# Kernel tuning notes

Measured on AMD Instinct MI355X. Metric: run time of the kernel, lower is better.

Reference implementation:

```python
import jax, jax.numpy as jnp
import numpy as np

# graph constants
B, V, CG, K, H, IN = 4, 6250, 25000, 3, 64, 2
NUM_LIT = B * 2 * V          # 50_000 literal nodes
NUM_CLS = B * CG             # 100_000 clause nodes
E = K * NUM_CLS              # 300_000 (l2c, c2l) edge pairs
NUM_ROUND = 3
DEMON = float(np.sqrt(H))    # self.demon = sqrt(hidden_size)


def setup_inputs() -> dict:
    key = jax.random.key(0)
    ks = jax.random.split(key, 12)
    rng = np.random.default_rng(0)
    # each clause has K literal endpoints; edges stay inside their own graph
    cls_idx = np.repeat(np.arange(NUM_CLS), K)
    g = cls_idx // CG
    lit_idx = g * 2 * V + rng.integers(0, 2 * V, size=E)

    def lin(k, fi, fo):
        return (jax.random.normal(k, (fi, fo), jnp.float32) / np.sqrt(fi)).astype(jnp.float32)

    return {
        "feat_l2c": jax.random.normal(ks[0], (E, IN), jnp.float32),
        "feat_c2l": jax.random.normal(ks[1], (E, IN), jnp.float32),
        "lit_idx": jnp.asarray(lit_idx, jnp.int32),
        "cls_idx": jnp.asarray(cls_idx, jnp.int32),
        "W_l2c_init": lin(ks[2], IN, H), "b_l2c_init": jnp.zeros((H,), jnp.float32),
        "W_c2l_init": lin(ks[3], IN, H), "b_c2l_init": jnp.zeros((H,), jnp.float32),
        "msgl_W": (jax.random.normal(ks[4], (3, H, H), jnp.float32) / np.sqrt(H)).astype(jnp.float32),
        "msgl_b": jnp.zeros((3, H), jnp.float32),
        "merge_W0": lin(ks[5], 2 * H, H), "merge_b0": jnp.zeros((H,), jnp.float32),
        "merge_Wr": (jax.random.normal(ks[6], (2, H, H), jnp.float32) / np.sqrt(H)).astype(jnp.float32),
        "merge_br": jnp.zeros((2, H), jnp.float32),
        "msgc_W": (jax.random.normal(ks[7], (3, H, H), jnp.float32) / np.sqrt(H)).astype(jnp.float32),
        "msgc_b": jnp.zeros((3, H), jnp.float32),
        "ro_W": (jax.random.normal(ks[8], (2, H, H), jnp.float32) / np.sqrt(H)).astype(jnp.float32),
        "ro_b": jnp.zeros((2, H), jnp.float32),
        "ro_W2": lin(ks[9], H, 1), "ro_b2": jnp.zeros((1,), jnp.float32),
    }


def _mlp3(x, W, b):  # 3-layer MLP, ReLU between layers (num_fc = 3)
    x = jax.nn.relu(x @ W[0] + b[0])
    x = jax.nn.relu(x @ W[1] + b[1])
    return x @ W[2] + b[2]


def reference(feat_l2c, feat_c2l, lit_idx, cls_idx,
              W_l2c_init, b_l2c_init, W_c2l_init, b_c2l_init,
              msgl_W, msgl_b, merge_W0, merge_b0, merge_Wr, merge_br,
              msgc_W, msgc_b, ro_W, ro_b, ro_W2, ro_b2):
    # init edge embeddings (l2c_init / c2l_init linear layers)
    h_l2c = feat_l2c @ W_l2c_init + b_l2c_init   # [E, H]
    h_c2l = feat_c2l @ W_c2l_init + b_c2l_init   # [E, H]

    for _ in range(NUM_ROUND):
        # literal update: aggregate incoming c2l messages, exclude self edge (BP-style)
        agg_l = jax.ops.segment_sum(h_c2l, lit_idx, num_segments=NUM_LIT)   # [NUM_LIT, H]
        m = _mlp3((agg_l[lit_idx] - h_c2l) / DEMON, msgl_W, msgl_b)          # [E, H]
        x = jax.nn.relu(jnp.concatenate([m, h_l2c], axis=-1) @ merge_W0 + merge_b0)
        x = jax.nn.relu(x @ merge_Wr[0] + merge_br[0])
        h_l2c = x @ merge_Wr[1] + merge_br[1]                                # l2c_merge_update
        # clause update
        agg_c = jax.ops.segment_sum(h_l2c, cls_idx, num_segments=NUM_CLS)   # [NUM_CLS, H]
        h_c2l = _mlp3((agg_c[cls_idx] - h_l2c) / DEMON, msgc_W, msgc_b)

    # u_add_e_sum with zero node feats == scatter-add edge emb to dst;
    # literal nodes only receive c2l edges
    l_emb = jax.ops.segment_sum(h_c2l, lit_idx, num_segments=NUM_LIT)        # [NUM_LIT, H]
    # segment_reduce(num_variable*2, ..., 'mean') over per-graph literal blocks (uniform sizes)
    l_mean = l_emb.reshape(B, 2 * V, H).mean(axis=1)                          # [B, H]
    x = jax.nn.relu(l_mean @ ro_W[0] + ro_b[0])
    x = jax.nn.relu(x @ ro_W[1] + ro_b[1])
    return jax.nn.sigmoid(x @ ro_W2 + ro_b2).squeeze(-1)                      # [B]
```

## Files before the change

kernel.cpp:

```cpp
#include <hip/hip_runtime.h>
#include <hip/hip_bf16.h>
#include <stdint.h>

#define EDGES   300000
#define NLIT    50000
#define NGRAPH  4
#define EPG     75000
#define HDIM    64

#define OFF_HL2C   0
#define OFF_HC2L   38400000
#define OFF_AGG    76800000
#define OFF_WT     89600000
#define OFF_ROACC  89681920
#define OFF_CNT    89682944
#define OFF_CSROFF 89882944
#define OFF_CURSOR 90082948
#define OFF_EIDX   90282948
#define OFF_BSUM   91482948
#define OFF_BBASE  91484000

#define WT_TOTAL    40960
#define WT_CLS_ELEM 28672

#define LIT_WBYTES (7 * 8192)
#define CLS_WBYTES (3 * 8192)
#define EPB2       256
#define NCHUNK     ((EDGES + EPB2 - 1) / EPB2)
#define LIT_GRID   512
#define CLS_GRID   1024

#define SCAN_BLOCKS ((NLIT + 255) / 256)

typedef __attribute__((ext_vector_type(8)))  short          s16x8;
typedef __attribute__((ext_vector_type(8)))  unsigned short u16x8;
typedef __attribute__((ext_vector_type(4)))  unsigned short u16x4;
typedef __attribute__((ext_vector_type(4)))  float          f32x4;
typedef __attribute__((ext_vector_type(16))) float          f32x16;

__device__ __forceinline__ f32x16 mfma32(s16x8 a, s16x8 b, f32x16 c) {
    return __builtin_amdgcn_mfma_f32_32x32x16_bf16(a, b, c, 0, 0, 0);
}
__device__ __forceinline__ float bf2f(unsigned short s) {
    union { unsigned int u; float f; } v; v.u = ((unsigned int)s) << 16; return v.f;
}
__device__ __forceinline__ unsigned short f2bf(float f) {
    union { __hip_bfloat16 b; unsigned short s; } v;
    v.b = __float2bfloat16(f);
    return v.s;
}
__device__ __forceinline__ unsigned pk2(float a, float b) {
    return (unsigned)f2bf(a) | ((unsigned)f2bf(b) << 16);
}

__device__ __forceinline__ void layer32(const char* __restrict__ unitBase,
                                        const float* __restrict__ biasL,
                                        const s16x8 (&bin)[4], f32x16 (&acc)[2],
                                        int eL, int hi)
{
#pragma unroll
    for (int t = 0; t < 2; ++t)
#pragma unroll
        for (int g = 0; g < 4; ++g) {
            f32x4 bv = *(const f32x4*)(biasL + 32 * t + 8 * g + 4 * hi);
#pragma unroll
            for (int r = 0; r < 4; ++r) acc[t][4 * g + r] = bv[r];
        }
#pragma unroll
    for (int kb = 0; kb < 4; ++kb)
#pragma unroll
        for (int t = 0; t < 2; ++t) {
            int row = 32 * t + eL;
            s16x8 a = *(const s16x8*)(unitBase + row * 128 +
                                      ((32 * kb + 16 * hi) ^ ((row & 7) << 4)));
            acc[t] = mfma32(a, bin[kb], acc[t]);
        }
}

template<bool RELU>
__device__ __forceinline__ void relayout32(f32x16 (&acc)[2], s16x8 (&bout)[4],
                                           int bpidx, int hi)
{
    if (RELU) {
#pragma unroll
        for (int t = 0; t < 2; ++t)
#pragma unroll
            for (int i = 0; i < 16; ++i) acc[t][i] = fmaxf(acc[t][i], 0.f);
    }
#pragma unroll
    for (int kb = 0; kb < 4; ++kb) {
        int m0 = 2 * kb, m1 = 2 * kb + 1;
        int t0 = m0 >> 2, g0 = m0 & 3, t1 = m1 >> 2, g1 = m1 & 3;
        unsigned A0 = pk2(acc[t0][4 * g0 + 0], acc[t0][4 * g0 + 1]);
        unsigned A1 = pk2(acc[t0][4 * g0 + 2], acc[t0][4 * g0 + 3]);
        unsigned B0 = pk2(acc[t1][4 * g1 + 0], acc[t1][4 * g1 + 1]);
        unsigned B1 = pk2(acc[t1][4 * g1 + 2], acc[t1][4 * g1 + 3]);
        unsigned pA0 = (unsigned)__builtin_amdgcn_ds_bpermute(bpidx, (int)A0);
        unsigned pA1 = (unsigned)__builtin_amdgcn_ds_bpermute(bpidx, (int)A1);
        unsigned pB0 = (unsigned)__builtin_amdgcn_ds_bpermute(bpidx, (int)B0);
        unsigned pB1 = (unsigned)__builtin_amdgcn_ds_bpermute(bpidx, (int)B1);
        union { unsigned w[4]; s16x8 v; } u;
        u.w[0] = hi ? pB0 : A0;
        u.w[1] = hi ? pB1 : A1;
        u.w[2] = hi ? B0 : pA0;
        u.w[3] = hi ? B1 : pA1;
        bout[kb] = u.v;
    }
}

__device__ __forceinline__ void store32(const f32x16 (&acc)[2],
                                        unsigned short* __restrict__ dst, int hi)
{
#pragma unroll
    for (int t = 0; t < 2; ++t)
#pragma unroll
        for (int g = 0; g < 4; ++g) {
            u16x4 p;
#pragma unroll
            for (int r = 0; r < 4; ++r) p[r] = f2bf(acc[t][4 * g + r]);
            *(u16x4*)(dst + 32 * t + 8 * g + 4 * hi) = p;
        }
}

__global__ __launch_bounds__(256) void prep_weights(
    const float* __restrict__ msgl_W, const float* __restrict__ merge_W0,
    const float* __restrict__ merge_Wr, const float* __restrict__ msgc_W,
    unsigned short* __restrict__ wT)
{
    int gid = blockIdx.x * 256 + threadIdx.x;
    if (gid >= WT_TOTAL) return;
    int unit = gid >> 12;
    int o = (gid >> 6) & 63;
    int csw = gid & 63;
    int i = csw ^ ((o & 7) << 3);
    float v;
    if (unit < 3)       v = msgl_W[unit * 4096 + i * 64 + o];
    else if (unit < 5)  v = merge_W0[((unit - 3) * 64 + i) * 64 + o];
    else if (unit < 7)  v = merge_Wr[(unit - 5) * 4096 + i * 64 + o];
    else                v = msgc_W[(unit - 7) * 4096 + i * 64 + o];
    wT[gid] = f2bf(v);
}

__global__ __launch_bounds__(256) void csr_hist(const int* __restrict__ lit_idx,
                                                int* __restrict__ cnt)
{
    int e = blockIdx.x * 256 + threadIdx.x;
    if (e < EDGES) atomicAdd(&cnt[lit_idx[e]], 1);
}

__global__ __launch_bounds__(256) void scan1(const int* __restrict__ cnt,
                                             int* __restrict__ bsum)
{
    __shared__ int red[4];
    int i = blockIdx.x * 256 + threadIdx.x;
    int s = (i < NLIT) ? cnt[i] : 0;
#pragma unroll
    for (int off = 1; off < 64; off <<= 1) s += __shfl_xor(s, off, 64);
    if ((threadIdx.x & 63) == 0) red[threadIdx.x >> 6] = s;
    __syncthreads();
    if (threadIdx.x == 0) bsum[blockIdx.x] = red[0] + red[1] + red[2] + red[3];
}

__global__ __launch_bounds__(256) void scan2(const int* __restrict__ bsum,
                                             int* __restrict__ bbase)
{
    __shared__ int tmp[256];
    int t = threadIdx.x;
    int v = (t < SCAN_BLOCKS) ? bsum[t] : 0;
    tmp[t] = v;
    __syncthreads();
#pragma unroll
    for (int off = 1; off < 256; off <<= 1) {
        int add = (t >= off) ? tmp[t - off] : 0;
        __syncthreads();
        tmp[t] += add;
        __syncthreads();
    }
    if (t < SCAN_BLOCKS) bbase[t] = tmp[t] - v;
}

__global__ __launch_bounds__(256) void scan3(const int* __restrict__ cnt,
                                             const int* __restrict__ bbase,
                                             int* __restrict__ off,
                                             int* __restrict__ cursor)
{
    __shared__ int tmp[256];
    int t = threadIdx.x;
    int i = blockIdx.x * 256 + t;
    int v = (i < NLIT) ? cnt[i] : 0;
    tmp[t] = v;
    __syncthreads();
#pragma unroll
    for (int offs = 1; offs < 256; offs <<= 1) {
        int add = (t >= offs) ? tmp[t - offs] : 0;
        __syncthreads();
        tmp[t] += add;
        __syncthreads();
    }
    if (i < NLIT) {
        int ex = bbase[blockIdx.x] + tmp[t] - v;
        off[i] = ex; cursor[i] = ex;
    }
    if (i == NLIT - 1) off[NLIT] = EDGES;
}

__global__ __launch_bounds__(256) void csr_scatter(const int* __restrict__ lit_idx,
                                                   int* __restrict__ cursor,
                                                   int* __restrict__ eidx)
{
    int e = blockIdx.x * 256 + threadIdx.x;
    if (e >= EDGES) return;
    int pos = atomicAdd(&cursor[lit_idx[e]], 1);
    eidx[pos] = e;
}

__global__ __launch_bounds__(256) void aggregate(const unsigned short* __restrict__ h_c2l,
                                                 const int* __restrict__ off,
                                                 const int* __restrict__ eidx,
                                                 float* __restrict__ agg)
{
    int t = threadIdx.x;
    int lane8 = t & 7;
    int lit = blockIdx.x * 32 + (t >> 3);
    if (lit >= NLIT) return;
    int lo = off[lit], hi = off[lit + 1];
    float s[8] = {0, 0, 0, 0, 0, 0, 0, 0};
    for (int i = lo; i < hi; ++i) {
        int e = eidx[i];
        u16x8 hv = *(const u16x8*)(h_c2l + e * 64 + lane8 * 8);
#pragma unroll
        for (int j = 0; j < 8; ++j) s[j] += bf2f(hv[j]);
    }
    f32x4 a0, a1;
    a0[0] = s[0]; a0[1] = s[1]; a0[2] = s[2]; a0[3] = s[3];
    a1[0] = s[4]; a1[1] = s[5]; a1[2] = s[6]; a1[3] = s[7];
    *(f32x4*)(agg + lit * 64 + lane8 * 8)     = a0;
    *(f32x4*)(agg + lit * 64 + lane8 * 8 + 4) = a1;
}

__global__ __launch_bounds__(256) void init_kernel(
    const float* __restrict__ feat_l2c, const float* __restrict__ feat_c2l,
    const float* __restrict__ W_l2c, const float* __restrict__ b_l2c,
    const float* __restrict__ W_c2l, const float* __restrict__ b_c2l,
    unsigned short* __restrict__ h_l2c, unsigned short* __restrict__ h_c2l)
{
    int gid = blockIdx.x * 256 + threadIdx.x;
    if (gid >= EDGES * 8) return;
    int e = gid >> 3, fo = (gid & 7) << 3;
    float2 fl = *(const float2*)(feat_l2c + e * 2);
    float2 fc = *(const float2*)(feat_c2l + e * 2);

    u16x8 outl, outc;
#pragma unroll
    for (int j = 0; j < 8; ++j) {
        float wl0 = W_l2c[fo + j], wl1 = W_l2c[64 + fo + j];
        float wc0 = W_c2l[fo + j], wc1 = W_c2l[64 + fo + j];
        float vl = fl.x * wl0 + fl.y * wl1 + b_l2c[fo + j];
        float vc = fc.x * wc0 + fc.y * wc1 + b_c2l[fo + j];
        outl[j] = f2bf(vl);
        outc[j] = f2bf(vc);
    }
    *(u16x8*)(h_l2c + e * 64 + fo) = outl;
    *(u16x8*)(h_c2l + e * 64 + fo) = outc;
}

__global__ __launch_bounds__(512, 4) void lit_update(
    const unsigned short* __restrict__ h_c2l,
    unsigned short* __restrict__ h_l2c,
    const float* __restrict__ agg,
    const int* __restrict__ lit_idx,
    const unsigned short* __restrict__ wT,
    const float* __restrict__ msgl_b,
    const float* __restrict__ merge_b0,
    const float* __restrict__ merge_br)
{
    __shared__ __align__(16) char lds[LIT_WBYTES + 384 * 4];
    int tid = threadIdx.x;
#pragma unroll
    for (int c = 0; c < 7; ++c) {
        int idx = c * 512 + tid;
        *(u16x8*)(lds + idx * 16) = *(const u16x8*)(wT + idx * 8);
    }
    float* ldsBias = (float*)(lds + LIT_WBYTES);
    if (tid < 384) {
        float v;
        if (tid < 192)      v = msgl_b[tid];
        else if (tid < 256) v = merge_b0[tid - 192];
        else                v = merge_br[tid - 256];
        ldsBias[tid] = v;
    }
    __syncthreads();

    int wv = tid >> 6, lane = tid & 63;
    int eL = lane & 31, hi = lane >> 5;
    int bpidx = (lane ^ 32) << 2;

    for (int c = blockIdx.x; c < NCHUNK; c += LIT_GRID) {
        int base = c * EPB2 + wv * 32;
        if (base >= EDGES) continue;
        int e = base + eL;
        int lit = lit_idx[e];

        s16x8 hfrag[4];
#pragma unroll
        for (int k = 0; k < 4; ++k)
            hfrag[k] = *(const s16x8*)(h_l2c + e * 64 + 16 * k + 8 * hi);

        s16x8 binp[4];
#pragma unroll
        for (int k = 0; k < 4; ++k) {
            int f0 = 16 * k + 8 * hi;
            f32x4 a0 = *(const f32x4*)(agg + lit * 64 + f0);
            f32x4 a1 = *(const f32x4*)(agg + lit * 64 + f0 + 4);
            u16x8 hv = *(const u16x8*)(h_c2l + e * 64 + f0);
            s16x8 b;
#pragma unroll
            for (int j = 0; j < 4; ++j) b[j]     = (short)f2bf((a0[j] - bf2f(hv[j]))     * 0.125f);
#pragma unroll
            for (int j = 0; j < 4; ++j) b[4 + j] = (short)f2bf((a1[j] - bf2f(hv[4 + j])) * 0.125f);
            binp[k] = b;
        }

        f32x16 acc[2];
        s16x8 bf[4];
        layer32(lds,            ldsBias,       binp, acc, eL, hi);
        relayout32<true >(acc, bf, bpidx, hi);
        layer32(lds + 8192,     ldsBias + 64,  bf, acc, eL, hi);
        relayout32<true >(acc, bf, bpidx, hi);
        layer32(lds + 2 * 8192, ldsBias + 128, bf, acc, eL, hi);
        relayout32<false>(acc, bf, bpidx, hi);

#pragma unroll
        for (int t = 0; t < 2; ++t)
#pragma unroll
            for (int g = 0; g < 4; ++g) {
                f32x4 bv = *(const f32x4*)(ldsBias + 192 + 32 * t + 8 * g + 4 * hi);
#pragma unroll
                for (int r = 0; r < 4; ++r) acc[t][4 * g + r] = bv[r];
            }
#pragma unroll
        for (int kb = 0; kb < 8; ++kb) {
            const char* ub = lds + (3 + (kb >> 2)) * 8192;
            s16x8 bop = (kb < 4) ? bf[kb] : hfrag[kb - 4];
#pragma unroll
            for (int t = 0; t < 2; ++t) {
                int row = 32 * t + eL;
                s16x8 a = *(const s16x8*)(ub + row * 128 +
                                          ((32 * (kb & 3) + 16 * hi) ^ ((row & 7) << 4)));
                acc[t] = mfma32(a, bop, acc[t]);
            }
        }
        relayout32<true>(acc, bf, bpidx, hi);
        layer32(lds + 5 * 8192, ldsBias + 256, bf, acc, eL, hi);
        relayout32<true>(acc, bf, bpidx, hi);
        layer32(lds + 6 * 8192, ldsBias + 320, bf, acc, eL, hi);

        store32(acc, h_l2c + e * 64, hi);
    }
}

__global__ __launch_bounds__(512, 4) void clause_update(
    const unsigned short* __restrict__ h_l2c,
    unsigned short* __restrict__ h_c2l,
    const unsigned short* __restrict__ msgcT,
    const float* __restrict__ msgc_b)
{
    __shared__ __align__(16) char lds[CLS_WBYTES + 192 * 4];
    int tid = threadIdx.x;
#pragma unroll
    for (int c = 0; c < 3; ++c) {
        int idx = c * 512 + tid;
        *(u16x8*)(lds + idx * 16) = *(const u16x8*)(msgcT + idx * 8);
    }
    float* ldsBias = (float*)(lds + CLS_WBYTES);
    if (tid < 192) ldsBias[tid] = msgc_b[tid];
    __syncthreads();

    int wv = tid >> 6, lane = tid & 63;
    int eL = lane & 31, hi = lane >> 5;
    int bpidx = (lane ^ 32) << 2;

    for (int c = blockIdx.x; c < NCHUNK; c += CLS_GRID) {
        int base = c * EPB2 + wv * 32;
        if (base >= EDGES) continue;
        int e = base + eL;

        int c3 = (e / 3) * 3;
        int d = e - c3;
        int e1 = c3 + (d == 0 ? 1 : 0);
        int e2 = c3 + (d == 2 ? 1 : 2);

        s16x8 binp[4];
#pragma unroll
        for (int k = 0; k < 4; ++k) {
            int f0 = 16 * k + 8 * hi;
            u16x8 h1 = *(const u16x8*)(h_l2c + e1 * 64 + f0);
            u16x8 h2 = *(const u16x8*)(h_l2c + e2 * 64 + f0);
            s16x8 b;
#pragma unroll
            for (int j = 0; j < 8; ++j)
                b[j] = (short)f2bf((bf2f(h1[j]) + bf2f(h2[j])) * 0.125f);
            binp[k] = b;
        }

        f32x16 acc[2];
        s16x8 bf[4];
        layer32(lds,            ldsBias,       binp, acc, eL, hi);
        relayout32<true>(acc, bf, bpidx, hi);
        layer32(lds + 8192,     ldsBias + 64,  bf, acc, eL, hi);
        relayout32<true>(acc, bf, bpidx, hi);
        layer32(lds + 2 * 8192, ldsBias + 128, bf, acc, eL, hi);

        store32(acc, h_c2l + e * 64, hi);
    }
}

__global__ __launch_bounds__(256) void readout_sum(
    const unsigned short* __restrict__ h_c2l, float* __restrict__ ro_acc)
{
    __shared__ float lsum[32][64];
    int g = blockIdx.x >> 6, chunk = blockIdx.x & 63;
    int t = threadIdx.x;
    int fg = t & 7, el = t >> 3;
    float s[8] = {0, 0, 0, 0, 0, 0, 0, 0};
    for (int idx = chunk * 32 + el; idx < EPG; idx += 2048) {
        u16x8 hv = *(const u16x8*)(h_c2l + (g * EPG + idx) * 64 + fg * 8);
#pragma unroll
        for (int j = 0; j < 8; ++j) s[j] += bf2f(hv[j]);
    }
#pragma unroll
    for (int j = 0; j < 8; ++j) lsum[el][fg * 8 + j] = s[j];
    __syncthreads();
    if (t < 64) {
        float tot = 0.f;
#pragma unroll 8
        for (int r = 0; r < 32; ++r) tot += lsum[r][t];
        atomicAdd(&ro_acc[g * 64 + t], tot);
    }
}

__global__ __launch_bounds__(256) void readout_mlp(
    const float* __restrict__ ro_acc, const float* __restrict__ ro_W,
    const float* __restrict__ ro_b, const float* __restrict__ ro_W2,
    const float* __restrict__ ro_b2, float* __restrict__ out)
{
    __shared__ float xb[NGRAPH][HDIM];
    __shared__ float yb[NGRAPH][HDIM];
    int g = threadIdx.x >> 6;
    int j = threadIdx.x & 63;
    xb[g][j] = ro_acc[g * HDIM + j] * (1.0f / 12500.0f);
    __syncthreads();
    float a = ro_b[j];
#pragma unroll 8
    for (int k = 0; k < HDIM; ++k) a += xb[g][k] * ro_W[k * HDIM + j];
    a = fmaxf(a, 0.0f);
    yb[g][j] = a;
    __syncthreads();
    float a2 = ro_b[HDIM + j];
#pragma unroll 8
    for (int k = 0; k < HDIM; ++k) a2 += yb[g][k] * ro_W[4096 + k * HDIM + j];
    a2 = fmaxf(a2, 0.0f);
    float p = a2 * ro_W2[j];
#pragma unroll
    for (int off = 32; off > 0; off >>= 1) p += __shfl_down(p, off, 64);
    if (j == 0) out[g] = 1.0f / (1.0f + expf(-(p + ro_b2[0])));
}

extern "C" void kernel_launch(void* const* d_in, const int* in_sizes, int n_in,
                              void* d_out, int out_size, void* d_ws, size_t ws_size,
                              hipStream_t stream)
{
    const float* feat_l2c = (const float*)d_in[0];
    const float* feat_c2l = (const float*)d_in[1];
    const int*   lit_idx  = (const int*)d_in[2];
    const float* W_l2c    = (const float*)d_in[4];
    const float* b_l2c    = (const float*)d_in[5];
    const float* W_c2l    = (const float*)d_in[6];
    const float* b_c2l    = (const float*)d_in[7];
    const float* msgl_W   = (const float*)d_in[8];
    const float* msgl_b   = (const float*)d_in[9];
    const float* merge_W0 = (const float*)d_in[10];
    const float* merge_b0 = (const float*)d_in[11];
    const float* merge_Wr = (const float*)d_in[12];
    const float* merge_br = (const float*)d_in[13];
    const float* msgc_W   = (const float*)d_in[14];
    const float* msgc_b   = (const float*)d_in[15];
    const float* ro_W     = (const float*)d_in[16];
    const float* ro_b     = (const float*)d_in[17];
    const float* ro_W2    = (const float*)d_in[18];
    const float* ro_b2    = (const float*)d_in[19];

    char* ws = (char*)d_ws;
    unsigned short* h_l2c  = (unsigned short*)(ws + OFF_HL2C);
    unsigned short* h_c2l  = (unsigned short*)(ws + OFF_HC2L);
    float*          agg    = (float*)(ws + OFF_AGG);
    unsigned short* wT     = (unsigned short*)(ws + OFF_WT);
    float*          ro_acc = (float*)(ws + OFF_ROACC);
    int*            cnt    = (int*)(ws + OFF_CNT);
    int*            csroff = (int*)(ws + OFF_CSROFF);
    int*            cursor = (int*)(ws + OFF_CURSOR);
    int*            eidx   = (int*)(ws + OFF_EIDX);
    int*            bsum   = (int*)(ws + OFF_BSUM);
    int*            bbase  = (int*)(ws + OFF_BBASE);

    hipMemsetAsync(cnt, 0, NLIT * sizeof(int), stream);
    hipMemsetAsync(ro_acc, 0, NGRAPH * 64 * sizeof(float), stream);

    prep_weights<<<(WT_TOTAL + 255) / 256, 256, 0, stream>>>(msgl_W, merge_W0, merge_Wr, msgc_W, wT);

    csr_hist<<<(EDGES + 255) / 256, 256, 0, stream>>>(lit_idx, cnt);
    scan1<<<SCAN_BLOCKS, 256, 0, stream>>>(cnt, bsum);
    scan2<<<1, 256, 0, stream>>>(bsum, bbase);
    scan3<<<SCAN_BLOCKS, 256, 0, stream>>>(cnt, bbase, csroff, cursor);
    csr_scatter<<<(EDGES + 255) / 256, 256, 0, stream>>>(lit_idx, cursor, eidx);

    init_kernel<<<EDGES * 8 / 256, 256, 0, stream>>>(feat_l2c, feat_c2l, W_l2c, b_l2c,
                                                     W_c2l, b_c2l, h_l2c, h_c2l);
    for (int r = 0; r < 3; ++r) {
        aggregate<<<(NLIT + 31) / 32, 256, 0, stream>>>(h_c2l, csroff, eidx, agg);
        lit_update<<<LIT_GRID, 512, 0, stream>>>(h_c2l, h_l2c, agg, lit_idx, wT,
                                                 msgl_b, merge_b0, merge_br);
        clause_update<<<CLS_GRID, 512, 0, stream>>>(h_l2c, h_c2l, wT + WT_CLS_ELEM, msgc_b);
    }
    readout_sum<<<256, 256, 0, stream>>>(h_c2l, ro_acc);
    readout_mlp<<<1, 256, 0, stream>>>(ro_acc, ro_W, ro_b, ro_W2, ro_b2, (float*)d_out);
}
```

Measured before the change: 341.6 us.

## Process two edge tiles per wave in lit_update and flatten grid loops

lit_update now has each wave handle two 32-edge tiles, sharing every LDS weight fragment load across two MFMA chains. Its launch bound drops to 3 blocks per CU to make room for the extra registers. Both update kernels switch from grid-stride loops to one chunk per block with a larger grid. relayout32 halves its ds_bpermute count by selecting the value to send before the permute, and the aggregate gather loop is unrolled by four to put more loads in flight. The higher register pressure in lit_update may lower occupancy or cause spills.

```diff
diff --git a/kernel.cpp b/kernel.cpp
--- a/kernel.cpp
+++ b/kernel.cpp
@@ -25,10 +25,10 @@
 
 #define LIT_WBYTES (7 * 8192)
 #define CLS_WBYTES (3 * 8192)
-#define EPB2       256
-#define NCHUNK     ((EDGES + EPB2 - 1) / EPB2)
-#define LIT_GRID   512
-#define CLS_GRID   1024
+#define LIT_EPB    512
+#define LIT_GRID   ((EDGES + LIT_EPB - 1) / LIT_EPB)
+#define CLS_EPB    256
+#define CLS_GRID   ((EDGES + CLS_EPB - 1) / CLS_EPB)
 
 #define SCAN_BLOCKS ((NLIT + 255) / 256)
 
@@ -51,30 +51,6 @@
 }
 __device__ __forceinline__ unsigned pk2(float a, float b) {
     return (unsigned)f2bf(a) | ((unsigned)f2bf(b) << 16);
-}
-
-__device__ __forceinline__ void layer32(const char* __restrict__ unitBase,
-                                        const float* __restrict__ biasL,
-                                        const s16x8 (&bin)[4], f32x16 (&acc)[2],
-                                        int eL, int hi)
-{
-#pragma unroll
-    for (int t = 0; t < 2; ++t)
-#pragma unroll
-        for (int g = 0; g < 4; ++g) {
-            f32x4 bv = *(const f32x4*)(biasL + 32 * t + 8 * g + 4 * hi);
-#pragma unroll
-            for (int r = 0; r < 4; ++r) acc[t][4 * g + r] = bv[r];
-        }
-#pragma unroll
-    for (int kb = 0; kb < 4; ++kb)
-#pragma unroll
-        for (int t = 0; t < 2; ++t) {
-            int row = 32 * t + eL;
-            s16x8 a = *(const s16x8*)(unitBase + row * 128 +
-                                      ((32 * kb + 16 * hi) ^ ((row & 7) << 4)));
-            acc[t] = mfma32(a, bin[kb], acc[t]);
-        }
 }
 
 template<bool RELU>
@@ -95,15 +71,15 @@
         unsigned A1 = pk2(acc[t0][4 * g0 + 2], acc[t0][4 * g0 + 3]);
         unsigned B0 = pk2(acc[t1][4 * g1 + 0], acc[t1][4 * g1 + 1]);
         unsigned B1 = pk2(acc[t1][4 * g1 + 2], acc[t1][4 * g1 + 3]);
-        unsigned pA0 = (unsigned)__builtin_amdgcn_ds_bpermute(bpidx, (int)A0);
-        unsigned pA1 = (unsigned)__builtin_amdgcn_ds_bpermute(bpidx, (int)A1);
-        unsigned pB0 = (unsigned)__builtin_amdgcn_ds_bpermute(bpidx, (int)B0);
-        unsigned pB1 = (unsigned)__builtin_amdgcn_ds_bpermute(bpidx, (int)B1);
+        unsigned s0 = hi ? A0 : B0;
+        unsigned s1 = hi ? A1 : B1;
+        unsigned p0 = (unsigned)__builtin_amdgcn_ds_bpermute(bpidx, (int)s0);
+        unsigned p1 = (unsigned)__builtin_amdgcn_ds_bpermute(bpidx, (int)s1);
         union { unsigned w[4]; s16x8 v; } u;
-        u.w[0] = hi ? pB0 : A0;
-        u.w[1] = hi ? pB1 : A1;
-        u.w[2] = hi ? B0 : pA0;
-        u.w[3] = hi ? B1 : pA1;
+        u.w[0] = hi ? p0 : A0;
+        u.w[1] = hi ? p1 : A1;
+        u.w[2] = hi ? B0 : p0;
+        u.w[3] = hi ? B1 : p1;
         bout[kb] = u.v;
     }
 }
@@ -119,6 +95,56 @@
 #pragma unroll
             for (int r = 0; r < 4; ++r) p[r] = f2bf(acc[t][4 * g + r]);
             *(u16x4*)(dst + 32 * t + 8 * g + 4 * hi) = p;
+        }
+}
+
+__device__ __forceinline__ void layer32(const char* __restrict__ unitBase,
+                                        const float* __restrict__ biasL,
+                                        const s16x8 (&bin)[4], f32x16 (&acc)[2],
+                                        int eL, int hi)
+{
+#pragma unroll
+    for (int t = 0; t < 2; ++t)
+#pragma unroll
+        for (int g = 0; g < 4; ++g) {
+            f32x4 bv = *(const f32x4*)(biasL + 32 * t + 8 * g + 4 * hi);
+#pragma unroll
+            for (int r = 0; r < 4; ++r) acc[t][4 * g + r] = bv[r];
+        }
+#pragma unroll
+    for (int kb = 0; kb < 4; ++kb)
+#pragma unroll
+        for (int t = 0; t < 2; ++t) {
+            int row = 32 * t + eL;
+            s16x8 a = *(const s16x8*)(unitBase + row * 128 +
+                                      ((32 * kb + 16 * hi) ^ ((row & 7) << 4)));
+            acc[t] = mfma32(a, bin[kb], acc[t]);
+        }
+}
+
+__device__ __forceinline__ void layer32x2(const char* __restrict__ unitBase,
+                                          const float* __restrict__ biasL,
+                                          const s16x8 (&b0)[4], const s16x8 (&b1)[4],
+                                          f32x16 (&acc0)[2], f32x16 (&acc1)[2],
+                                          int eL, int hi)
+{
+#pragma unroll
+    for (int t = 0; t < 2; ++t)
+#pragma unroll
+        for (int g = 0; g < 4; ++g) {
+            f32x4 bv = *(const f32x4*)(biasL + 32 * t + 8 * g + 4 * hi);
+#pragma unroll
+            for (int r = 0; r < 4; ++r) { acc0[t][4 * g + r] = bv[r]; acc1[t][4 * g + r] = bv[r]; }
+        }
+#pragma unroll
+    for (int kb = 0; kb < 4; ++kb)
+#pragma unroll
+        for (int t = 0; t < 2; ++t) {
+            int row = 32 * t + eL;
+            s16x8 a = *(const s16x8*)(unitBase + row * 128 +
+                                      ((32 * kb + 16 * hi) ^ ((row & 7) << 4)));
+            acc0[t] = mfma32(a, b0[kb], acc0[t]);
+            acc1[t] = mfma32(a, b1[kb], acc1[t]);
         }
 }
 
@@ -225,7 +251,18 @@
     if (lit >= NLIT) return;
     int lo = off[lit], hi = off[lit + 1];
     float s[8] = {0, 0, 0, 0, 0, 0, 0, 0};
-    for (int i = lo; i < hi; ++i) {
+    int i = lo;
+    for (; i + 4 <= hi; i += 4) {
+        int e0 = eidx[i], e1 = eidx[i + 1], e2 = eidx[i + 2], e3 = eidx[i + 3];
+        u16x8 v0 = *(const u16x8*)(h_c2l + e0 * 64 + lane8 * 8);
+        u16x8 v1 = *(const u16x8*)(h_c2l + e1 * 64 + lane8 * 8);
+        u16x8 v2 = *(const u16x8*)(h_c2l + e2 * 64 + lane8 * 8);
+        u16x8 v3 = *(const u16x8*)(h_c2l + e3 * 64 + lane8 * 8);
+#pragma unroll
+        for (int j = 0; j < 8; ++j)
+            s[j] += (bf2f(v0[j]) + bf2f(v1[j])) + (bf2f(v2[j]) + bf2f(v3[j]));
+    }
+    for (; i < hi; ++i) {
         int e = eidx[i];
         u16x8 hv = *(const u16x8*)(h_c2l + e * 64 + lane8 * 8);
 #pragma unroll
@@ -264,7 +301,7 @@
     *(u16x8*)(h_c2l + e * 64 + fo) = outc;
 }
 
-__global__ __launch_bounds__(512, 4) void lit_update(
+__global__ __launch_bounds__(512, 3) void lit_update(
     const unsigned short* __restrict__ h_c2l,
     unsigned short* __restrict__ h_l2c,
     const float* __restrict__ agg,
@@ -294,69 +331,86 @@
     int wv = tid >> 6, lane = tid & 63;
     int eL = lane & 31, hi = lane >> 5;
     int bpidx = (lane ^ 32) << 2;
-
-    for (int c = blockIdx.x; c < NCHUNK; c += LIT_GRID) {
-        int base = c * EPB2 + wv * 32;
-        if (base >= EDGES) continue;
-        int e = base + eL;
-        int lit = lit_idx[e];
-
-        s16x8 hfrag[4];
-#pragma unroll
-        for (int k = 0; k < 4; ++k)
-            hfrag[k] = *(const s16x8*)(h_l2c + e * 64 + 16 * k + 8 * hi);
-
-        s16x8 binp[4];
-#pragma unroll
-        for (int k = 0; k < 4; ++k) {
-            int f0 = 16 * k + 8 * hi;
-            f32x4 a0 = *(const f32x4*)(agg + lit * 64 + f0);
-            f32x4 a1 = *(const f32x4*)(agg + lit * 64 + f0 + 4);
-            u16x8 hv = *(const u16x8*)(h_c2l + e * 64 + f0);
-            s16x8 b;
-#pragma unroll
-            for (int j = 0; j < 4; ++j) b[j]     = (short)f2bf((a0[j] - bf2f(hv[j]))     * 0.125f);
-#pragma unroll
-            for (int j = 0; j < 4; ++j) b[4 + j] = (short)f2bf((a1[j] - bf2f(hv[4 + j])) * 0.125f);
-            binp[k] = b;
-        }
-
-        f32x16 acc[2];
-        s16x8 bf[4];
-        layer32(lds,            ldsBias,       binp, acc, eL, hi);
-        relayout32<true >(acc, bf, bpidx, hi);
-        layer32(lds + 8192,     ldsBias + 64,  bf, acc, eL, hi);
-        relayout32<true >(acc, bf, bpidx, hi);
-        layer32(lds + 2 * 8192, ldsBias + 128, bf, acc, eL, hi);
-        relayout32<false>(acc, bf, bpidx, hi);
-
-#pragma unroll
-        for (int t = 0; t < 2; ++t)
-#pragma unroll
-            for (int g = 0; g < 4; ++g) {
-                f32x4 bv = *(const f32x4*)(ldsBias + 192 + 32 * t + 8 * g + 4 * hi);
-#pragma unroll
-                for (int r = 0; r < 4; ++r) acc[t][4 * g + r] = bv[r];
-            }
-#pragma unroll
-        for (int kb = 0; kb < 8; ++kb) {
-            const char* ub = lds + (3 + (kb >> 2)) * 8192;
-            s16x8 bop = (kb < 4) ? bf[kb] : hfrag[kb - 4];
-#pragma unroll
-            for (int t = 0; t < 2; ++t) {
-                int row = 32 * t + eL;
-                s16x8 a = *(const s16x8*)(ub + row * 128 +
-                                          ((32 * (kb & 3) + 16 * hi) ^ ((row & 7) << 4)));
-                acc[t] = mfma32(a, bop, acc[t]);
-            }
-        }
-        relayout32<true>(acc, bf, bpidx, hi);
-        layer32(lds + 5 * 8192, ldsBias + 256, bf, acc, eL, hi);
-        relayout32<true>(acc, bf, bpidx, hi);
-        layer32(lds + 6 * 8192, ldsBias + 320, bf, acc, eL, hi);
-
-        store32(acc, h_l2c + e * 64, hi);
-    }
+    int base = blockIdx.x * LIT_EPB + wv * 64;
+    if (base >= EDGES) return;
+    bool has2 = (base + 32) < EDGES;
+    int e0 = base + eL;
+    int e1 = has2 ? (base + 32 + eL) : e0;
+    int l0 = lit_idx[e0];
+    int l1 = lit_idx[e1];
+
+    s16x8 hfragA[4], hfragB[4];
+#pragma unroll
+    for (int k = 0; k < 4; ++k) {
+        hfragA[k] = *(const s16x8*)(h_l2c + e0 * 64 + 16 * k + 8 * hi);
+        hfragB[k] = *(const s16x8*)(h_l2c + e1 * 64 + 16 * k + 8 * hi);
+    }
+
+    s16x8 bfA[4], bfB[4];
+#pragma unroll
+    for (int k = 0; k < 4; ++k) {
+        int f0 = 16 * k + 8 * hi;
+        f32x4 a0 = *(const f32x4*)(agg + l0 * 64 + f0);
+        f32x4 a1 = *(const f32x4*)(agg + l0 * 64 + f0 + 4);
+        u16x8 hv = *(const u16x8*)(h_c2l + e0 * 64 + f0);
+        s16x8 b;
+#pragma unroll
+        for (int j = 0; j < 4; ++j) b[j]     = (short)f2bf((a0[j] - bf2f(hv[j]))     * 0.125f);
+#pragma unroll
+        for (int j = 0; j < 4; ++j) b[4 + j] = (short)f2bf((a1[j] - bf2f(hv[4 + j])) * 0.125f);
+        bfA[k] = b;
+        f32x4 c0 = *(const f32x4*)(agg + l1 * 64 + f0);
+        f32x4 c1 = *(const f32x4*)(agg + l1 * 64 + f0 + 4);
+        u16x8 hw = *(const u16x8*)(h_c2l + e1 * 64 + f0);
+#pragma unroll
+        for (int j = 0; j < 4; ++j) b[j]     = (short)f2bf((c0[j] - bf2f(hw[j]))     * 0.125f);
+#pragma unroll
+        for (int j = 0; j < 4; ++j) b[4 + j] = (short)f2bf((c1[j] - bf2f(hw[4 + j])) * 0.125f);
+        bfB[k] = b;
+    }
+
+    f32x16 accA[2], accB[2];
+    layer32x2(lds,            ldsBias,       bfA, bfB, accA, accB, eL, hi);
+    relayout32<true >(accA, bfA, bpidx, hi);
+    relayout32<true >(accB, bfB, bpidx, hi);
+    layer32x2(lds + 8192,     ldsBias + 64,  bfA, bfB, accA, accB, eL, hi);
+    relayout32<true >(accA, bfA, bpidx, hi);
+    relayout32<true >(accB, bfB, bpidx, hi);
+    layer32x2(lds + 2 * 8192, ldsBias + 128, bfA, bfB, accA, accB, eL, hi);
+    relayout32<false>(accA, bfA, bpidx, hi);
+    relayout32<false>(accB, bfB, bpidx, hi);
+
+#pragma unroll
+    for (int t = 0; t < 2; ++t)
+#pragma unroll
+        for (int g = 0; g < 4; ++g) {
+            f32x4 bv = *(const f32x4*)(ldsBias + 192 + 32 * t + 8 * g + 4 * hi);
+#pragma unroll
+            for (int r = 0; r < 4; ++r) { accA[t][4 * g + r] = bv[r]; accB[t][4 * g + r] = bv[r]; }
+        }
+#pragma unroll
+    for (int kb = 0; kb < 8; ++kb) {
+        const char* ub = lds + (3 + (kb >> 2)) * 8192;
+        s16x8 bA = (kb < 4) ? bfA[kb] : hfragA[kb - 4];
+        s16x8 bB = (kb < 4) ? bfB[kb] : hfragB[kb - 4];
+#pragma unroll
+        for (int t = 0; t < 2; ++t) {
+            int row = 32 * t + eL;
+            s16x8 a = *(const s16x8*)(ub + row * 128 +
+                                      ((32 * (kb & 3) + 16 * hi) ^ ((row & 7) << 4)));
+            accA[t] = mfma32(a, bA, accA[t]);
+            accB[t] = mfma32(a, bB, accB[t]);
+        }
+    }
+    relayout32<true>(accA, bfA, bpidx, hi);
+    relayout32<true>(accB, bfB, bpidx, hi);
+    layer32x2(lds + 5 * 8192, ldsBias + 256, bfA, bfB, accA, accB, eL, hi);
+    relayout32<true>(accA, bfA, bpidx, hi);
+    relayout32<true>(accB, bfB, bpidx, hi);
+    layer32x2(lds + 6 * 8192, ldsBias + 320, bfA, bfB, accA, accB, eL, hi);
+
+    store32(accA, h_l2c + e0 * 64, hi);
+    if (has2) store32(accB, h_l2c + e1 * 64, hi);
 }
 
 __global__ __launch_bounds__(512, 4) void clause_update(
@@ -379,40 +433,37 @@
     int wv = tid >> 6, lane = tid & 63;
     int eL = lane & 31, hi = lane >> 5;
     int bpidx = (lane ^ 32) << 2;
-
-    for (int c = blockIdx.x; c < NCHUNK; c += CLS_GRID) {
-        int base = c * EPB2 + wv * 32;
-        if (base >= EDGES) continue;
-        int e = base + eL;
-
-        int c3 = (e / 3) * 3;
-        int d = e - c3;
-        int e1 = c3 + (d == 0 ? 1 : 0);
-        int e2 = c3 + (d == 2 ? 1 : 2);
-
-        s16x8 binp[4];
-#pragma unroll
-        for (int k = 0; k < 4; ++k) {
-            int f0 = 16 * k + 8 * hi;
-            u16x8 h1 = *(const u16x8*)(h_l2c + e1 * 64 + f0);
-            u16x8 h2 = *(const u16x8*)(h_l2c + e2 * 64 + f0);
-            s16x8 b;
-#pragma unroll
-            for (int j = 0; j < 8; ++j)
-                b[j] = (short)f2bf((bf2f(h1[j]) + bf2f(h2[j])) * 0.125f);
-            binp[k] = b;
-        }
-
-        f32x16 acc[2];
-        s16x8 bf[4];
-        layer32(lds,            ldsBias,       binp, acc, eL, hi);
-        relayout32<true>(acc, bf, bpidx, hi);
-        layer32(lds + 8192,     ldsBias + 64,  bf, acc, eL, hi);
-        relayout32<true>(acc, bf, bpidx, hi);
-        layer32(lds + 2 * 8192, ldsBias + 128, bf, acc, eL, hi);
-
-        store32(acc, h_c2l + e * 64, hi);
-    }
+    int base = blockIdx.x * CLS_EPB + wv * 32;
+    if (base >= EDGES) return;
+    int e = base + eL;
+
+    int c3 = (e / 3) * 3;
+    int d = e - c3;
+    int e1 = c3 + (d == 0 ? 1 : 0);
+    int e2 = c3 + (d == 2 ? 1 : 2);
+
+    s16x8 binp[4];
+#pragma unroll
+    for (int k = 0; k < 4; ++k) {
+        int f0 = 16 * k + 8 * hi;
+        u16x8 h1 = *(const u16x8*)(h_l2c + e1 * 64 + f0);
+        u16x8 h2 = *(const u16x8*)(h_l2c + e2 * 64 + f0);
+        s16x8 b;
+#pragma unroll
+        for (int j = 0; j < 8; ++j)
+            b[j] = (short)f2bf((bf2f(h1[j]) + bf2f(h2[j])) * 0.125f);
+        binp[k] = b;
+    }
+
+    f32x16 acc[2];
+    s16x8 bf[4];
+    layer32(lds,            ldsBias,       binp, acc, eL, hi);
+    relayout32<true>(acc, bf, bpidx, hi);
+    layer32(lds + 8192,     ldsBias + 64,  bf, acc, eL, hi);
+    relayout32<true>(acc, bf, bpidx, hi);
+    layer32(lds + 2 * 8192, ldsBias + 128, bf, acc, eL, hi);
+
+    store32(acc, h_c2l + e * 64, hi);
 }
 
 __global__ __launch_bounds__(256) void readout_sum(
```

After: 378.4 us. 10.8% more time.
